# Kernel optimization log

Measured on AMD Instinct MI355X. Metric: run time of the kernel, lower is better.

## Reference

```python
import jax, jax.numpy as jnp
import numpy as np

B, S, E, FF = 8, 16384, 256, 1024
H, W, G = 128, 128, 16
Hn, Wn = H // G, W // G


def setup_inputs() -> dict:
    key = jax.random.key(0)
    ks = jax.random.split(key, 16)
    w = lambda k, shape: jax.random.normal(k, shape, jnp.float32) * 0.02
    return {
        "x": jax.random.normal(ks[0], (B, S, E), jnp.float32),
        "Wq": w(ks[1], (E, E)), "bq": jnp.zeros((E,), jnp.float32),
        "Wk": w(ks[2], (E, E)), "bk": jnp.zeros((E,), jnp.float32),
        "Wv": w(ks[3], (E, E)), "bv": jnp.zeros((E,), jnp.float32),
        "Wo": w(ks[4], (E, E)), "bo": jnp.zeros((E,), jnp.float32),
        "W1": w(ks[5], (E, FF)), "b1": jnp.zeros((FF,), jnp.float32),
        "W2": w(ks[6], (FF, E)), "b2": jnp.zeros((E,), jnp.float32),
        "g1": jnp.ones((E,), jnp.float32), "be1": jnp.zeros((E,), jnp.float32),
        "g2": jnp.ones((E,), jnp.float32), "be2": jnp.zeros((E,), jnp.float32),
    }


def _ln(x, g, b, eps=1e-5):
    m = jnp.mean(x, axis=-1, keepdims=True)
    v = jnp.mean(jnp.square(x - m), axis=-1, keepdims=True)
    return (x - m) * jax.lax.rsqrt(v + eps) * g + b


def _forward(x, Wq, bq, Wk, bk, Wv, bv, Wo, bo, W1, b1, W2, b2, g1, be1, g2, be2):
    # x: (B, S, E) -> (B, E, H, W), faithful to torch reshape (row-major reinterpret)
    x4 = x.reshape(B, E, H, W)
    # window partition: each window is the contiguous (E, G, G) block the torch loop slices
    xw = x4.reshape(B, E, Hn, G, Wn, G).transpose(0, 2, 4, 1, 3, 5)  # (B,Hn,Wn,E,G,G)
    # faithful raw reinterpretation (E,G,G) -> (G*G, E), matching grid.reshape(B,-1,E)
    t = xw.reshape(B, Hn * Wn, G * G, E)  # (B, nW, T=256, E)
    # single-head self-attention per window (batched over all windows at once)
    q = jnp.einsum('bwte,ef->bwtf', t, Wq) + bq
    k = jnp.einsum('bwte,ef->bwtf', t, Wk) + bk
    v = jnp.einsum('bwte,ef->bwtf', t, Wv) + bv
    scores = jnp.einsum('bwqe,bwke->bwqk', q, k) / jnp.sqrt(jnp.float32(E))
    attn = jax.nn.softmax(scores, axis=-1)
    o = jnp.einsum('bwqk,bwke->bwqe', attn, v)
    o = jnp.einsum('bwte,ef->bwtf', o, Wo) + bo  # (B, nW, 256, E)
    # reverse: view each window back to (E,G,G) and reassemble the feature map
    y = o.reshape(B, Hn, Wn, E, G, G).transpose(0, 3, 1, 4, 2, 5).reshape(B, E, H, W)
    y = y.reshape(B, S, E)  # faithful x.view(B, -1, E)
    # FFN (dropout is identity in eval) + residual with post-LN as written
    h = jax.nn.gelu(jnp.einsum('bse,ef->bsf', y, W1) + b1, approximate=False)
    ffn = jnp.einsum('bsf,fe->bse', h, W2) + b2
    y = y + _ln(ffn, g1, be1)
    y = y + _ln(y, g2, be2)
    return y


def reference(x, Wq, bq, Wk, bk, Wv, bv, Wo, bo, W1, b1, W2, b2, g1, be1, g2, be2):
    return _forward(x, Wq, bq, Wk, bk, Wv, bv, Wo, bo, W1, b1, W2, b2, g1, be1, g2, be2)
```

## Files before the change

### kernel.cpp

```cpp
#include <hip/hip_runtime.h>
#include <hip/hip_bf16.h>


typedef __bf16 bf16x8 __attribute__((ext_vector_type(8)));
typedef float  f32x4  __attribute__((ext_vector_type(4)));
typedef unsigned short us16;
typedef us16 us16x8 __attribute__((ext_vector_type(8)));
typedef us16 us16x4 __attribute__((ext_vector_type(4)));
typedef us16 us16x2 __attribute__((ext_vector_type(2)));

#define DI static __device__ __forceinline__

DI us16 f2b(float f){ __bf16 h = (__bf16)f; return __builtin_bit_cast(us16, h); }

DI bf16x8 cvt8(f32x4 a, f32x4 b){
  bf16x8 r;
  r[0]=(__bf16)a[0]; r[1]=(__bf16)a[1]; r[2]=(__bf16)a[2]; r[3]=(__bf16)a[3];
  r[4]=(__bf16)b[0]; r[5]=(__bf16)b[1]; r[6]=(__bf16)b[2]; r[7]=(__bf16)b[3];
  return r;
}
DI bf16x8 ld8(const us16* p){
  us16x8 v = *(const us16x8*)p;
  return __builtin_bit_cast(bf16x8, v);
}
DI f32x4 mfma16(bf16x8 a, bf16x8 b, f32x4 c){
  return __builtin_amdgcn_mfma_f32_16x16x32_bf16(a, b, c, 0, 0, 0);
}

DI bf16x8 ld_sw8(const char* base, int row, int f0){
  return ld8((const us16*)(base + row*512 + ((((f0>>3) ^ (row&7))) << 4)));
}
DI void st_sw1(char* base, int row, int f, us16 v){
  *(us16*)(base + row*512 + ((((f>>3) ^ (row&7))) << 4) + (f&7)*2) = v;
}
DI void st_sw4(char* base, int row, int f0, us16x4 v){
  *(us16x4*)(base + row*512 + ((((f0>>3) ^ (row&7))) << 4) + (f0&7)*2) = v;
}

DI bf16x8 ld_vt(const char* base, int row, int gg){
  return ld8((const us16*)(base + row*64 + (((gg ^ ((row>>1)&3))) << 4)));
}
DI void st_vt(char* base, int row, int col, us16 v){
  int c = col >> 3;
  *(us16*)(base + row*64 + (((c ^ ((row>>1)&3))) << 4) + (col&7)*2) = v;
}

DI void st_h1s(char* base, int row, int f, us16 v){
  *(us16*)(base + row*2048 + ((((f>>3) ^ (row&7))) << 4) + (f&7)*2) = v;
}
DI bf16x8 ld_h8s(const char* base, int row, int f0){
  return ld8((const us16*)(base + row*2048 + ((((f0>>3) ^ (row&7))) << 4)));
}

__global__ void prep_w(const float* __restrict__ src, us16* __restrict__ dst,
                       int R, int C, int cshift){
  int idx = blockIdx.x*256 + threadIdx.x;
  if(idx >= R*C) return;
  int r = idx >> cshift;
  int c = idx & (C-1);
  dst[(size_t)c*R + r] = f2b(src[idx]);
}

__global__ __launch_bounds__(256, 2)
void qkv_win(const float* __restrict__ x,
             const us16* __restrict__ WqT, const us16* __restrict__ WkT,
             const us16* __restrict__ WvT,
             const float* __restrict__ bq, const float* __restrict__ bk,
             const float* __restrict__ bv,
             char* __restrict__ Qimg, char* __restrict__ KV)
{
  __shared__ __align__(16) char smem[65536];
  const int tid = threadIdx.x;
  const int wl = tid >> 6, lane = tid & 63, l15 = lane & 15, g = lane >> 4;
  const int blk = blockIdx.x;
  const int hw = blk & 1, tg = (blk>>1)&7, wh = (blk>>4)&7, b = blk>>7;
  const int win = wh*8 + hw*4 + wl;

  {
    const float* xb = x + (size_t)b*4194304 + (size_t)(tg*32)*16384 + wh*2048 + hw*64;
    const int prow = tid >> 4, pc = tid & 15;
    char* abase = smem + (pc>>2)*16384;
    const int f0 = prow*16 + (pc&3)*4;
    for(int t=0; t<32; t++){
      f32x4 v = *(const f32x4*)(xb + (size_t)t*16384 + prow*128 + pc*4);
      us16x4 pk; pk[0]=f2b(v[0]); pk[1]=f2b(v[1]); pk[2]=f2b(v[2]); pk[3]=f2b(v[3]);
      st_sw4(abase, t, f0, pk);
    }
  }
  __syncthreads();
  bf16x8 tA[2][8];
  #pragma unroll
  for(int mi=0; mi<2; mi++)
    #pragma unroll
    for(int kk=0; kk<8; kk++)
      tA[mi][kk] = ld_sw8(smem + wl*16384, mi*16 + l15, kk*32 + g*8);
  __syncthreads();

  char* outb = smem + wl*16384;
  const size_t wslot = (size_t)(b*64 + win);

  for(int n0=0; n0<16; n0++){
    f32x4 a0 = {0,0,0,0}, a1 = {0,0,0,0};
    const us16* wrow = WqT + (size_t)(n0*16 + l15)*256;
    #pragma unroll
    for(int kk=0; kk<8; kk++){
      bf16x8 wb = ld8(wrow + kk*32 + g*8);
      a0 = mfma16(tA[0][kk], wb, a0);
      a1 = mfma16(tA[1][kk], wb, a1);
    }
    float bias = bq[n0*16 + l15];
    #pragma unroll
    for(int r=0; r<4; r++){
      st_sw1(outb, g*4+r,    n0*16+l15, f2b(a0[r] + bias));
      st_sw1(outb, 16+g*4+r, n0*16+l15, f2b(a1[r] + bias));
    }
  }
  asm volatile("" ::: "memory");
  {
    char* dst = Qimg + (wslot*8 + tg)*16384;
    #pragma unroll
    for(int i=0; i<16; i++)
      *(us16x8*)(dst + i*1024 + lane*16) = *(const us16x8*)(outb + i*1024 + lane*16);
  }
  asm volatile("" ::: "memory");

  for(int n0=0; n0<16; n0++){
    f32x4 a0 = {0,0,0,0}, a1 = {0,0,0,0};
    const us16* wrow = WkT + (size_t)(n0*16 + l15)*256;
    #pragma unroll
    for(int kk=0; kk<8; kk++){
      bf16x8 wb = ld8(wrow + kk*32 + g*8);
      a0 = mfma16(tA[0][kk], wb, a0);
      a1 = mfma16(tA[1][kk], wb, a1);
    }
    float bias = bk[n0*16 + l15];
    #pragma unroll
    for(int r=0; r<4; r++){
      st_sw1(outb, g*4+r,    n0*16+l15, f2b(a0[r] + bias));
      st_sw1(outb, 16+g*4+r, n0*16+l15, f2b(a1[r] + bias));
    }
  }
  asm volatile("" ::: "memory");
  {
    char* dst = KV + wslot*262144 + tg*16384;
    #pragma unroll
    for(int i=0; i<16; i++)
      *(us16x8*)(dst + i*1024 + lane*16) = *(const us16x8*)(outb + i*1024 + lane*16);
  }
  asm volatile("" ::: "memory");

  for(int n0=0; n0<16; n0++){
    f32x4 a0 = {0,0,0,0}, a1 = {0,0,0,0};
    const us16* wrow = WvT + (size_t)(n0*16 + l15)*256;
    f32x4 bv4 = *(const f32x4*)(bv + n0*16 + g*4);
    #pragma unroll
    for(int kk=0; kk<8; kk++){
      bf16x8 wa = ld8(wrow + kk*32 + g*8);
      a0 = mfma16(wa, tA[0][kk], a0);
      a1 = mfma16(wa, tA[1][kk], a1);
    }
    #pragma unroll
    for(int r=0; r<4; r++){
      int jr = n0*16 + g*4 + r;
      st_vt(outb, jr, l15,      f2b(a0[r] + bv4[r]));
      st_vt(outb, jr, 16 + l15, f2b(a1[r] + bv4[r]));
    }
  }
  asm volatile("" ::: "memory");
  {
    char* dst = KV + wslot*262144 + 131072 + tg*16384;
    #pragma unroll
    for(int i=0; i<16; i++)
      *(us16x8*)(dst + i*1024 + lane*16) = *(const us16x8*)(outb + i*1024 + lane*16);
  }
}

__global__ __launch_bounds__(256, 2)
void kv_win(const float* __restrict__ x,
            const us16* __restrict__ WkT, const us16* __restrict__ WvT,
            const float* __restrict__ bk, const float* __restrict__ bv,
            char* __restrict__ KV)
{
  __shared__ __align__(16) char smem[65536];
  const int tid = threadIdx.x;
  const int wl = tid >> 6, lane = tid & 63, l15 = lane & 15, g = lane >> 4;
  const int blk = blockIdx.x;
  const int hw = blk & 1, tg = (blk>>1)&7, wh = (blk>>4)&7, b = blk>>7;
  const int win = wh*8 + hw*4 + wl;

  {
    const float* xb = x + (size_t)b*4194304 + (size_t)(tg*32)*16384 + wh*2048 + hw*64;
    const int prow = tid >> 4, pc = tid & 15;
    char* abase = smem + (pc>>2)*16384;
    const int f0 = prow*16 + (pc&3)*4;
    for(int t=0; t<32; t++){
      f32x4 v = *(const f32x4*)(xb + (size_t)t*16384 + prow*128 + pc*4);
      us16x4 pk; pk[0]=f2b(v[0]); pk[1]=f2b(v[1]); pk[2]=f2b(v[2]); pk[3]=f2b(v[3]);
      st_sw4(abase, t, f0, pk);
    }
  }
  __syncthreads();
  bf16x8 tA[2][8];
  #pragma unroll
  for(int mi=0; mi<2; mi++)
    #pragma unroll
    for(int kk=0; kk<8; kk++)
      tA[mi][kk] = ld_sw8(smem + wl*16384, mi*16 + l15, kk*32 + g*8);
  __syncthreads();

  char* outb = smem + wl*16384;
  const size_t wslot = (size_t)(b*64 + win);

  for(int n0=0; n0<16; n0++){
    f32x4 a0 = {0,0,0,0}, a1 = {0,0,0,0};
    const us16* wrow = WkT + (size_t)(n0*16 + l15)*256;
    #pragma unroll
    for(int kk=0; kk<8; kk++){
      bf16x8 wb = ld8(wrow + kk*32 + g*8);
      a0 = mfma16(tA[0][kk], wb, a0);
      a1 = mfma16(tA[1][kk], wb, a1);
    }
    float bias = bk[n0*16 + l15];
    #pragma unroll
    for(int r=0; r<4; r++){
      st_sw1(outb, g*4+r,    n0*16+l15, f2b(a0[r] + bias));
      st_sw1(outb, 16+g*4+r, n0*16+l15, f2b(a1[r] + bias));
    }
  }
  asm volatile("" ::: "memory");
  {
    char* dst = KV + wslot*262144 + tg*16384;
    #pragma unroll
    for(int i=0; i<16; i++)
      *(us16x8*)(dst + i*1024 + lane*16) = *(const us16x8*)(outb + i*1024 + lane*16);
  }
  asm volatile("" ::: "memory");

  for(int n0=0; n0<16; n0++){
    f32x4 a0 = {0,0,0,0}, a1 = {0,0,0,0};
    const us16* wrow = WvT + (size_t)(n0*16 + l15)*256;
    f32x4 bv4 = *(const f32x4*)(bv + n0*16 + g*4);
    #pragma unroll
    for(int kk=0; kk<8; kk++){
      bf16x8 wa = ld8(wrow + kk*32 + g*8);
      a0 = mfma16(wa, tA[0][kk], a0);
      a1 = mfma16(wa, tA[1][kk], a1);
    }
    #pragma unroll
    for(int r=0; r<4; r++){
      int jr = n0*16 + g*4 + r;
      st_vt(outb, jr, l15,      f2b(a0[r] + bv4[r]));
      st_vt(outb, jr, 16 + l15, f2b(a1[r] + bv4[r]));
    }
  }
  asm volatile("" ::: "memory");
  {
    char* dst = KV + wslot*262144 + 131072 + tg*16384;
    #pragma unroll
    for(int i=0; i<16; i++)
      *(us16x8*)(dst + i*1024 + lane*16) = *(const us16x8*)(outb + i*1024 + lane*16);
  }
}

DI void load_kv_regs(const char* slot, int kt, us16x8* r, int wid, int lane){
  const char* src = (wid < 4)
      ? slot + (size_t)kt*16384 + wid*4096
      : slot + 131072 + (size_t)kt*16384 + (wid-4)*4096;
  #pragma unroll
  for(int i=0; i<4; i++)
    r[i] = *(const us16x8*)(src + i*1024 + lane*16);
}
DI void write_kv_lds(char* kb, char* vb, const us16x8* r, int wid, int lane){
  char* dst = (wid < 4) ? kb + wid*4096 : vb + (wid-4)*4096;
  #pragma unroll
  for(int i=0; i<4; i++)
    *(us16x8*)(dst + i*1024 + lane*16) = r[i];
}

DI void attn_core_loop(char* smem, us16* Psw, const char* slot,
                       const bf16x8 Qf[2][8], us16x8* stg,
                       const us16* WoT, const float* bo, float* yb,
                       int wid, int lane, int l15, int g, int r0)
{
  us16* Qw = (us16*)(smem) + wid*(32*264);
  float mr0 = -1e30f, mr1 = -1e30f, lr0 = 0.f, lr1 = 0.f;
  f32x4 Ot[16][2];
  const f32x4 zf = {0,0,0,0};
  #pragma unroll
  for(int i=0;i<16;i++){ Ot[i][0]=zf; Ot[i][1]=zf; }
  __syncthreads();

  for(int kt=0; kt<8; kt++){
    char* kb = (kt&1) ? smem + 16384 : smem;
    char* vb = (kt&1) ? smem + 49152 : smem + 32768;
    if(kt < 7) load_kv_regs(slot, kt+1, stg, wid, lane);
    f32x4 st[2][2] = {{zf,zf},{zf,zf}};
    #pragma unroll
    for(int kk=0; kk<8; kk++){
      int f0 = kk*32 + g*8;
      bf16x8 k0 = ld_sw8(kb, l15, f0);
      bf16x8 k1 = ld_sw8(kb, 16 + l15, f0);
      st[0][0] = mfma16(k0, Qf[0][kk], st[0][0]);
      st[0][1] = mfma16(k0, Qf[1][kk], st[0][1]);
      st[1][0] = mfma16(k1, Qf[0][kk], st[1][0]);
      st[1][1] = mfma16(k1, Qf[1][kk], st[1][1]);
    }
    #pragma unroll
    for(int mi=0; mi<2; mi++)
      #pragma unroll
      for(int qn=0; qn<2; qn++)
        #pragma unroll
        for(int r=0; r<4; r++) st[mi][qn][r] *= 0.0625f;
    float tm0 = st[0][0][0], tm1 = st[0][1][0];
    #pragma unroll
    for(int mi=0; mi<2; mi++)
      #pragma unroll
      for(int r=0; r<4; r++){
        tm0 = fmaxf(tm0, st[mi][0][r]);
        tm1 = fmaxf(tm1, st[mi][1][r]);
      }
    tm0 = fmaxf(tm0, __shfl_xor(tm0, 16)); tm0 = fmaxf(tm0, __shfl_xor(tm0, 32));
    tm1 = fmaxf(tm1, __shfl_xor(tm1, 16)); tm1 = fmaxf(tm1, __shfl_xor(tm1, 32));
    float mn0 = fmaxf(mr0, tm0), mn1 = fmaxf(mr1, tm1);
    float c0 = __expf(mr0 - mn0), c1 = __expf(mr1 - mn1);
    float ts0 = 0.f, ts1 = 0.f;
    #pragma unroll
    for(int mi=0; mi<2; mi++)
      #pragma unroll
      for(int r=0; r<4; r++){
        float p0 = __expf(st[mi][0][r] - mn0); st[mi][0][r] = p0; ts0 += p0;
        float p1 = __expf(st[mi][1][r] - mn1); st[mi][1][r] = p1; ts1 += p1;
      }
    ts0 += __shfl_xor(ts0, 16); ts0 += __shfl_xor(ts0, 32);
    ts1 += __shfl_xor(ts1, 16); ts1 += __shfl_xor(ts1, 32);
    lr0 = lr0*c0 + ts0;  lr1 = lr1*c1 + ts1;  mr0 = mn0;  mr1 = mn1;
    #pragma unroll
    for(int i=0;i<16;i++){
      #pragma unroll
      for(int r=0;r<4;r++){ Ot[i][0][r] *= c0; Ot[i][1][r] *= c1; }
    }
    #pragma unroll
    for(int qn=0; qn<2; qn++)
      #pragma unroll
      for(int mi=0; mi<2; mi++)
        #pragma unroll
        for(int rp=0; rp<2; rp++){
          us16x2 pk;
          pk[0] = f2b(st[mi][qn][rp*2]);
          pk[1] = f2b(st[mi][qn][rp*2+1]);
          *(us16x2*)((char*)Psw + (qn*16 + l15)*80 + (mi*16 + g*4 + rp*2)*2) = pk;
        }
    asm volatile("" ::: "memory");
    bf16x8 pb0 = ld8(Psw + l15*40 + g*8);
    bf16x8 pb1 = ld8(Psw + (16 + l15)*40 + g*8);
    #pragma unroll
    for(int fm=0; fm<16; fm++){
      bf16x8 va = ld_vt(vb, fm*16 + l15, g);
      Ot[fm][0] = mfma16(va, pb0, Ot[fm][0]);
      Ot[fm][1] = mfma16(va, pb1, Ot[fm][1]);
    }
    if(kt < 7){
      char* kbn = (kt&1) ? smem : smem + 16384;
      char* vbn = (kt&1) ? smem + 32768 : smem + 49152;
      write_kv_lds(kbn, vbn, stg, wid, lane);
    }
    __syncthreads();
  }

  float inv0 = 1.f/lr0, inv1 = 1.f/lr1;
  #pragma unroll
  for(int fm=0; fm<16; fm++)
    #pragma unroll
    for(int rp=0; rp<2; rp++){
      us16x2 p0, p1;
      p0[0]=f2b(Ot[fm][0][rp*2]*inv0);   p0[1]=f2b(Ot[fm][0][rp*2+1]*inv0);
      p1[0]=f2b(Ot[fm][1][rp*2]*inv1);   p1[1]=f2b(Ot[fm][1][rp*2+1]*inv1);
      *(us16x2*)((char*)Qw + l15*528      + (fm*16 + g*4 + rp*2)*2) = p0;
      *(us16x2*)((char*)Qw + (16+l15)*528 + (fm*16 + g*4 + rp*2)*2) = p1;
    }
  asm volatile("" ::: "memory");
  bf16x8 Of[2][8];
  #pragma unroll
  for(int qm=0; qm<2; qm++)
    #pragma unroll
    for(int kk=0; kk<8; kk++)
      Of[qm][kk] = ld8(Qw + (qm*16 + l15)*264 + kk*32 + g*8);
  for(int n0=0; n0<16; n0++){
    f32x4 a0 = {0,0,0,0}, a1 = {0,0,0,0};
    const us16* wrow = WoT + (size_t)(n0*16 + l15)*256;
    #pragma unroll
    for(int kk=0; kk<8; kk++){
      bf16x8 wb = ld8(wrow + kk*32 + g*8);
      a0 = mfma16(Of[0][kk], wb, a0);
      a1 = mfma16(Of[1][kk], wb, a1);
    }
    float bias = bo[n0*16 + l15];
    #pragma unroll
    for(int r=0; r<4; r++){
      yb[(size_t)(r0 + g*4 + r)*16384      + n0*128 + l15] = a0[r] + bias;
      yb[(size_t)(r0 + 16 + g*4 + r)*16384 + n0*128 + l15] = a1[r] + bias;
    }
  }
}

__global__ __launch_bounds__(512, 2)
void attn_hyb2(const char* __restrict__ Qimg, const char* __restrict__ KV,
               const us16* __restrict__ WoT, const float* __restrict__ bo,
               float* __restrict__ y)
{
  __shared__ __align__(16) char smem[135168];
  const int tid = threadIdx.x, wid = tid>>6, lane = tid&63, l15 = lane&15, g = lane>>4;
  const int blk = blockIdx.x;
  const int b   = blk >> 6;
  const int win = blk & 63;
  const size_t base = (size_t)b*4194304 + (size_t)(win>>3)*2048 + (size_t)(win&7)*16;
  float*       yb = y + base;
  const char*  slot = KV + (size_t)blk*262144;
  const char*  Qt = Qimg + ((size_t)blk*8 + wid)*16384;
  us16* Psw = (us16*)(smem + 65536) + wid*1280;
  const int r0 = wid*32;

  us16x8 stg[4];
  load_kv_regs(slot, 0, stg, wid, lane);

  bf16x8 Qf[2][8];
  #pragma unroll
  for(int qn=0; qn<2; qn++)
    #pragma unroll
    for(int kk=0; kk<8; kk++){
      int row = qn*16 + l15;
      Qf[qn][kk] = ld8((const us16*)(Qt + row*512 + ((((kk*4+g) ^ (l15&7))) << 4)));
    }

  write_kv_lds(smem, smem + 32768, stg, wid, lane);
  attn_core_loop(smem, Psw, slot, Qf, stg, WoT, bo, yb, wid, lane, l15, g, r0);
}

__global__ __launch_bounds__(512, 2)
void attn_hyb(const float* __restrict__ x,
              const us16* __restrict__ WqT, const float* __restrict__ bq,
              const char* __restrict__ KV,
              const us16* __restrict__ WoT, const float* __restrict__ bo,
              float* __restrict__ y)
{
  __shared__ __align__(16) char smem[135168];
  const int tid = threadIdx.x, wid = tid>>6, lane = tid&63, l15 = lane&15, g = lane>>4;
  const int blk = blockIdx.x;
  const int b   = blk >> 6;
  const int win = blk & 63;
  const size_t base = (size_t)b*4194304 + (size_t)(win>>3)*2048 + (size_t)(win&7)*16;
  const float* xb = x + base;
  float*       yb = y + base;
  const char*  slot = KV + (size_t)blk*262144;

  us16* Qw  = (us16*)(smem) + wid*(32*264);
  us16* Psw = (us16*)(smem + 65536) + wid*1280;
  const int r0 = wid*32;

  us16x8 stg[4];
  load_kv_regs(slot, 0, stg, wid, lane);

  bf16x8 tA[2][8];
  #pragma unroll
  for(int mi=0; mi<2; mi++){
    const float* trow = xb + (size_t)(r0 + mi*16 + l15)*16384;
    #pragma unroll
    for(int kk=0; kk<8; kk++){
      int f0 = kk*32 + g*8;
      const float* p = trow + (f0>>4)*128 + (f0&15);
      tA[mi][kk] = cvt8(*(const f32x4*)p, *(const f32x4*)(p+4));
    }
  }
  for(int n0=0; n0<16; n0++){
    f32x4 a0 = {0,0,0,0}, a1 = {0,0,0,0};
    const us16* wrow = WqT + (size_t)(n0*16 + l15)*256;
    #pragma unroll
    for(int kk=0; kk<8; kk++){
      bf16x8 wb = ld8(wrow + kk*32 + g*8);
      a0 = mfma16(tA[0][kk], wb, a0);
      a1 = mfma16(tA[1][kk], wb, a1);
    }
    float bias = bq[n0*16 + l15];
    #pragma unroll
    for(int r=0; r<4; r++){
      Qw[(g*4+r)*264      + n0*16 + l15] = f2b(a0[r] + bias);
      Qw[(16+g*4+r)*264   + n0*16 + l15] = f2b(a1[r] + bias);
    }
  }
  asm volatile("" ::: "memory");
  bf16x8 Qf[2][8];
  #pragma unroll
  for(int qn=0; qn<2; qn++)
    #pragma unroll
    for(int kk=0; kk<8; kk++)
      Qf[qn][kk] = ld8(Qw + (qn*16 + l15)*264 + kk*32 + g*8);
  __syncthreads();

  write_kv_lds(smem, smem + 32768, stg, wid, lane);
  attn_core_loop(smem, Psw, slot, Qf, stg, WoT, bo, yb, wid, lane, l15, g, r0);
}

__global__ __launch_bounds__(512, 2)
void ffn_ln(float* y,
            const us16* __restrict__ W1T, const us16* __restrict__ W2T,
            const float* __restrict__ b1, const float* __restrict__ b2,
            const float* __restrict__ g1, const float* __restrict__ be1,
            const float* __restrict__ g2, const float* __restrict__ be2)
{
  __shared__ __align__(16) char smem[132096];
  us16*  h  = (us16*)smem;
  float* fl = (float*)smem;
  const int tid = threadIdx.x, wid = tid>>6, lane = tid&63, l15 = lane&15, g = lane>>4;
  float* Y = y + (size_t)blockIdx.x*64*256;

  bf16x8 ya[4][8];
  #pragma unroll
  for(int mi=0; mi<4; mi++){
    const float* p = Y + (size_t)(mi*16 + l15)*256;
    #pragma unroll
    for(int kk=0; kk<8; kk++){
      int f0 = kk*32 + g*8;
      ya[mi][kk] = cvt8(*(const f32x4*)(p + f0), *(const f32x4*)(p + f0 + 4));
    }
  }
  const f32x4 zf = {0,0,0,0};
  #pragma unroll 2
  for(int n0=0; n0<8; n0++){
    int j = wid*128 + n0*16 + l15;
    f32x4 acc[4] = {zf,zf,zf,zf};
    const us16* wrow = W1T + (size_t)j*256;
    #pragma unroll
    for(int kk=0; kk<8; kk++){
      bf16x8 wb = ld8(wrow + kk*32 + g*8);
      #pragma unroll
      for(int mi=0; mi<4; mi++) acc[mi] = mfma16(ya[mi][kk], wb, acc[mi]);
    }
    float bias = b1[j];
    #pragma unroll
    for(int mi=0; mi<4; mi++)
      #pragma unroll
      for(int r=0; r<4; r++){
        float v = acc[mi][r] + bias;
        v = 0.5f*v*(1.f + erff(v*0.70710678118654752f));
        h[(mi*16 + g*4 + r)*1032 + j] = f2b(v);
      }
  }
  __syncthreads();
  f32x4 acc2[4][2] = {{zf,zf},{zf,zf},{zf,zf},{zf,zf}};
  #pragma unroll 2
  for(int kk=0; kk<32; kk++){
    int f0 = kk*32 + g*8;
    bf16x8 ha[4];
    #pragma unroll
    for(int mi=0; mi<4; mi++) ha[mi] = ld8(h + (mi*16 + l15)*1032 + f0);
    #pragma unroll
    for(int n=0; n<2; n++){
      bf16x8 wb = ld8(W2T + (size_t)(wid*32 + n*16 + l15)*1024 + f0);
      #pragma unroll
      for(int mi=0; mi<4; mi++) acc2[mi][n] = mfma16(ha[mi], wb, acc2[mi][n]);
    }
  }
  __syncthreads();
  #pragma unroll
  for(int mi=0; mi<4; mi++)
    #pragma unroll
    for(int n=0; n<2; n++){
      float bias = b2[wid*32 + n*16 + l15];
      #pragma unroll
      for(int r=0; r<4; r++)
        fl[(mi*16 + g*4 + r)*260 + wid*32 + n*16 + l15] = acc2[mi][n][r] + bias;
    }
  __syncthreads();
  f32x4 G1  = *(const f32x4*)(g1  + lane*4);
  f32x4 BE1 = *(const f32x4*)(be1 + lane*4);
  f32x4 G2  = *(const f32x4*)(g2  + lane*4);
  f32x4 BE2 = *(const f32x4*)(be2 + lane*4);
  for(int rr=0; rr<8; rr++){
    int row = wid*8 + rr;
    f32x4 f  = *(const f32x4*)(fl + row*260 + lane*4);
    f32x4 yv = *(const f32x4*)(Y + (size_t)row*256 + lane*4);
    float s  = f[0]+f[1]+f[2]+f[3];
    float s2 = f[0]*f[0]+f[1]*f[1]+f[2]*f[2]+f[3]*f[3];
    #pragma unroll
    for(int m=1; m<=32; m<<=1){ s += __shfl_xor(s, m); s2 += __shfl_xor(s2, m); }
    float mu = s*(1.f/256.f);
    float rs = rsqrtf(fmaxf(s2*(1.f/256.f) - mu*mu, 0.f) + 1e-5f);
    f32x4 y1;
    #pragma unroll
    for(int i=0; i<4; i++) y1[i] = yv[i] + (f[i]-mu)*rs*G1[i] + BE1[i];
    float t1 = y1[0]+y1[1]+y1[2]+y1[3];
    float t2 = y1[0]*y1[0]+y1[1]*y1[1]+y1[2]*y1[2]+y1[3]*y1[3];
    #pragma unroll
    for(int m=1; m<=32; m<<=1){ t1 += __shfl_xor(t1, m); t2 += __shfl_xor(t2, m); }
    float mu2 = t1*(1.f/256.f);
    float rs2 = rsqrtf(fmaxf(t2*(1.f/256.f) - mu2*mu2, 0.f) + 1e-5f);
    f32x4 o;
    #pragma unroll
    for(int i=0; i<4; i++) o[i] = y1[i] + (y1[i]-mu2)*rs2*G2[i] + BE2[i];
    *(f32x4*)(Y + (size_t)row*256 + lane*4) = o;
  }
}

__global__ __launch_bounds__(512, 2)
void ffn_ln32s(float* y,
               const us16* __restrict__ W1T, const us16* __restrict__ W2T,
               const float* __restrict__ b1, const float* __restrict__ b2,
               const float* __restrict__ g1, const float* __restrict__ be1,
               const float* __restrict__ g2, const float* __restrict__ be2)
{
  __shared__ __align__(16) char smem[65536];
  float* fl = (float*)smem;
  const int tid = threadIdx.x, wid = tid>>6, lane = tid&63, l15 = lane&15, g = lane>>4;
  float* Y = y + (size_t)blockIdx.x*32*256;

  bf16x8 ya[2][8];
  #pragma unroll
  for(int mi=0; mi<2; mi++){
    const float* p = Y + (size_t)(mi*16 + l15)*256;
    #pragma unroll
    for(int kk=0; kk<8; kk++){
      int f0 = kk*32 + g*8;
      ya[mi][kk] = cvt8(*(const f32x4*)(p + f0), *(const f32x4*)(p + f0 + 4));
    }
  }
  const f32x4 zf = {0,0,0,0};
  for(int n0=0; n0<8; n0++){
    int j = wid*128 + n0*16 + l15;
    f32x4 acc[2] = {zf,zf};
    const us16* wrow = W1T + (size_t)j*256;
    #pragma unroll
    for(int kk=0; kk<8; kk++){
      bf16x8 wb = ld8(wrow + kk*32 + g*8);
      #pragma unroll
      for(int mi=0; mi<2; mi++) acc[mi] = mfma16(ya[mi][kk], wb, acc[mi]);
    }
    float bias = b1[j];
    #pragma unroll
    for(int mi=0; mi<2; mi++)
      #pragma unroll
      for(int r=0; r<4; r++){
        float v = acc[mi][r] + bias;
        v = 0.5f*v*(1.f + erff(v*0.70710678118654752f));
        st_h1s(smem, mi*16 + g*4 + r, j, f2b(v));
      }
  }
  __syncthreads();
  f32x4 acc2[2][2] = {{zf,zf},{zf,zf}};
  for(int kk=0; kk<32; kk++){
    int f0 = kk*32 + g*8;
    bf16x8 ha[2];
    #pragma unroll
    for(int mi=0; mi<2; mi++) ha[mi] = ld_h8s(smem, mi*16 + l15, f0);
    #pragma unroll
    for(int n=0; n<2; n++){
      bf16x8 wb = ld8(W2T + (size_t)(wid*32 + n*16 + l15)*1024 + f0);
      #pragma unroll
      for(int mi=0; mi<2; mi++) acc2[mi][n] = mfma16(ha[mi], wb, acc2[mi][n]);
    }
  }
  __syncthreads();
  #pragma unroll
  for(int mi=0; mi<2; mi++)
    #pragma unroll
    for(int n=0; n<2; n++){
      float bias = b2[wid*32 + n*16 + l15];
      #pragma unroll
      for(int r=0; r<4; r++)
        fl[(mi*16 + g*4 + r)*260 + wid*32 + n*16 + l15] = acc2[mi][n][r] + bias;
    }
  __syncthreads();
  f32x4 G1  = *(const f32x4*)(g1  + lane*4);
  f32x4 BE1 = *(const f32x4*)(be1 + lane*4);
  f32x4 G2  = *(const f32x4*)(g2  + lane*4);
  f32x4 BE2 = *(const f32x4*)(be2 + lane*4);
  for(int rr=0; rr<4; rr++){
    int row = wid*4 + rr;
    f32x4 f  = *(const f32x4*)(fl + row*260 + lane*4);
    f32x4 yv = *(const f32x4*)(Y + (size_t)row*256 + lane*4);
    float s  = f[0]+f[1]+f[2]+f[3];
    float s2 = f[0]*f[0]+f[1]*f[1]+f[2]*f[2]+f[3]*f[3];
    #pragma unroll
    for(int m=1; m<=32; m<<=1){ s += __shfl_xor(s, m); s2 += __shfl_xor(s2, m); }
    float mu = s*(1.f/256.f);
    float rs = rsqrtf(fmaxf(s2*(1.f/256.f) - mu*mu, 0.f) + 1e-5f);
    f32x4 y1;
    #pragma unroll
    for(int i=0; i<4; i++) y1[i] = yv[i] + (f[i]-mu)*rs*G1[i] + BE1[i];
    float t1 = y1[0]+y1[1]+y1[2]+y1[3];
    float t2 = y1[0]*y1[0]+y1[1]*y1[1]+y1[2]*y1[2]+y1[3]*y1[3];
    #pragma unroll
    for(int m=1; m<=32; m<<=1){ t1 += __shfl_xor(t1, m); t2 += __shfl_xor(t2, m); }
    float mu2 = t1*(1.f/256.f);
    float rs2 = rsqrtf(fmaxf(t2*(1.f/256.f) - mu2*mu2, 0.f) + 1e-5f);
    f32x4 o;
    #pragma unroll
    for(int i=0; i<4; i++) o[i] = y1[i] + (y1[i]-mu2)*rs2*G2[i] + BE2[i];
    *(f32x4*)(Y + (size_t)row*256 + lane*4) = o;
  }
}

__global__ __launch_bounds__(512, 2)
void attn_win(const float* __restrict__ x,
              const us16* __restrict__ WqT, const us16* __restrict__ WkT,
              const us16* __restrict__ WvT, const us16* __restrict__ WoT,
              const float* __restrict__ bq, const float* __restrict__ bk,
              const float* __restrict__ bv, const float* __restrict__ bo,
              float* __restrict__ y)
{
  __shared__ __align__(16) char smem[135168];
  const int tid = threadIdx.x;
  const int wid = tid >> 6;
  const int lane = tid & 63;
  const int l15 = lane & 15;
  const int g = lane >> 4;

  const int blk = blockIdx.x;
  const int b   = blk >> 6;
  const int win = blk & 63;
  const size_t base = (size_t)b*4194304 + (size_t)(win>>3)*2048 + (size_t)(win&7)*16;
  const float* xb = x + base;
  float*       yb = y + base;

  us16* Qw    = (us16*)(smem) + wid*(32*264);
  char* slabb = smem;
  char* kldsb = smem + 16384;
  us16* Vt    = (us16*)(smem + 32768);
  us16* Psw   = (us16*)(smem + 53248) + wid*1280;

  const int r0 = wid*32;

  bf16x8 tA[2][8];
  #pragma unroll
  for(int mi=0; mi<2; mi++){
    const float* trow = xb + (size_t)(r0 + mi*16 + l15)*16384;
    #pragma unroll
    for(int kk=0; kk<8; kk++){
      int f0 = kk*32 + g*8;
      const float* p = trow + (f0>>4)*128 + (f0&15);
      tA[mi][kk] = cvt8(*(const f32x4*)p, *(const f32x4*)(p+4));
    }
  }
  for(int n0=0; n0<16; n0++){
    f32x4 a0 = {0,0,0,0}, a1 = {0,0,0,0};
    const us16* wrow = WqT + (size_t)(n0*16 + l15)*256;
    #pragma unroll
    for(int kk=0; kk<8; kk++){
      bf16x8 wb = ld8(wrow + kk*32 + g*8);
      a0 = mfma16(tA[0][kk], wb, a0);
      a1 = mfma16(tA[1][kk], wb, a1);
    }
    float bias = bq[n0*16 + l15];
    #pragma unroll
    for(int r=0; r<4; r++){
      Qw[(g*4+r)*264      + n0*16 + l15] = f2b(a0[r] + bias);
      Qw[(16+g*4+r)*264   + n0*16 + l15] = f2b(a1[r] + bias);
    }
  }
  asm volatile("" ::: "memory");
  bf16x8 Qf[2][8];
  #pragma unroll
  for(int qn=0; qn<2; qn++)
    #pragma unroll
    for(int kk=0; kk<8; kk++)
      Qf[qn][kk] = ld8(Qw + (qn*16 + l15)*264 + kk*32 + g*8);
  __syncthreads();

  const float bkv0 = bk[wid*32 + l15], bkv1 = bk[wid*32 + 16 + l15];
  float bvv[2][4];
  #pragma unroll
  for(int m=0; m<2; m++)
    #pragma unroll
    for(int r=0; r<4; r++)
      bvv[m][r] = bv[wid*32 + m*16 + g*4 + r];

  float mr0 = -1e30f, mr1 = -1e30f, lr0 = 0.f, lr1 = 0.f;
  f32x4 Ot[16][2];
  const f32x4 zf = {0,0,0,0};
  #pragma unroll
  for(int i=0;i<16;i++){ Ot[i][0]=zf; Ot[i][1]=zf; }

  for(int kt=0; kt<8; kt++){
    const int kr0 = kt*32;
    {
      int row = tid >> 4, c = tid & 15;
      const float* trow = xb + (size_t)(kr0 + row)*16384;
      #pragma unroll
      for(int j=0; j<4; j++){
        int f0 = (c + 16*j)*4;
        const float* p = trow + (f0>>4)*128 + (f0&15);
        f32x4 v = *(const f32x4*)p;
        us16x4 pk; pk[0]=f2b(v[0]); pk[1]=f2b(v[1]); pk[2]=f2b(v[2]); pk[3]=f2b(v[3]);
        st_sw4(slabb, row, f0, pk);
      }
    }
    __syncthreads();
    {
      f32x4 acc[2][2] = {{zf,zf},{zf,zf}};
      #pragma unroll
      for(int kk=0; kk<8; kk++){
        int f0 = kk*32 + g*8;
        bf16x8 a0 = ld_sw8(slabb, l15, f0);
        bf16x8 a1 = ld_sw8(slabb, 16 + l15, f0);
        #pragma unroll
        for(int n=0; n<2; n++){
          bf16x8 wb = ld8(WkT + (size_t)(wid*32 + n*16 + l15)*256 + f0);
          acc[n][0] = mfma16(a0, wb, acc[n][0]);
          acc[n][1] = mfma16(a1, wb, acc[n][1]);
        }
      }
      #pragma unroll
      for(int n=0; n<2; n++){
        float bias = n ? bkv1 : bkv0;
        #pragma unroll
        for(int r=0; r<4; r++){
          st_sw1(kldsb, g*4+r,      wid*32 + n*16 + l15, f2b(acc[n][0][r] + bias));
          st_sw1(kldsb, 16+g*4+r,   wid*32 + n*16 + l15, f2b(acc[n][1][r] + bias));
        }
      }
    }
    {
      f32x4 acc[2][2] = {{zf,zf},{zf,zf}};
      #pragma unroll
      for(int kk=0; kk<8; kk++){
        int f0 = kk*32 + g*8;
        bf16x8 b0 = ld_sw8(slabb, l15, f0);
        bf16x8 b1 = ld_sw8(slabb, 16 + l15, f0);
        #pragma unroll
        for(int fm=0; fm<2; fm++){
          bf16x8 wa = ld8(WvT + (size_t)(wid*32 + fm*16 + l15)*256 + f0);
          acc[fm][0] = mfma16(wa, b0, acc[fm][0]);
          acc[fm][1] = mfma16(wa, b1, acc[fm][1]);
        }
      }
      #pragma unroll
      for(int fm=0; fm<2; fm++)
        #pragma unroll
        for(int n=0; n<2; n++)
          #pragma unroll
          for(int r=0; r<4; r++){
            int f = wid*32 + fm*16 + g*4 + r;
            Vt[f*40 + n*16 + l15] = f2b(acc[fm][n][r] + bvv[fm][r]);
          }
    }
    __syncthreads();
    f32x4 st[2][2] = {{zf,zf},{zf,zf}};
    #pragma unroll
    for(int kk=0; kk<8; kk++){
      int f0 = kk*32 + g*8;
      bf16x8 k0 = ld_sw8(kldsb, l15, f0);
      bf16x8 k1 = ld_sw8(kldsb, 16 + l15, f0);
      st[0][0] = mfma16(k0, Qf[0][kk], st[0][0]);
      st[0][1] = mfma16(k0, Qf[1][kk], st[0][1]);
      st[1][0] = mfma16(k1, Qf[0][kk], st[1][0]);
      st[1][1] = mfma16(k1, Qf[1][kk], st[1][1]);
    }
    #pragma unroll
    for(int mi=0; mi<2; mi++)
      #pragma unroll
      for(int qn=0; qn<2; qn++)
        #pragma unroll
        for(int r=0; r<4; r++) st[mi][qn][r] *= 0.0625f;
    float tm0 = st[0][0][0], tm1 = st[0][1][0];
    #pragma unroll
    for(int mi=0; mi<2; mi++)
      #pragma unroll
      for(int r=0; r<4; r++){
        tm0 = fmaxf(tm0, st[mi][0][r]);
        tm1 = fmaxf(tm1, st[mi][1][r]);
      }
    tm0 = fmaxf(tm0, __shfl_xor(tm0, 16)); tm0 = fmaxf(tm0, __shfl_xor(tm0, 32));
    tm1 = fmaxf(tm1, __shfl_xor(tm1, 16)); tm1 = fmaxf(tm1, __shfl_xor(tm1, 32));
    float mn0 = fmaxf(mr0, tm0), mn1 = fmaxf(mr1, tm1);
    float c0 = __expf(mr0 - mn0), c1 = __expf(mr1 - mn1);
    float ts0 = 0.f, ts1 = 0.f;
    #pragma unroll
    for(int mi=0; mi<2; mi++)
      #pragma unroll
      for(int r=0; r<4; r++){
        float p0 = __expf(st[mi][0][r] - mn0); st[mi][0][r] = p0; ts0 += p0;
        float p1 = __expf(st[mi][1][r] - mn1); st[mi][1][r] = p1; ts1 += p1;
      }
    ts0 += __shfl_xor(ts0, 16); ts0 += __shfl_xor(ts0, 32);
    ts1 += __shfl_xor(ts1, 16); ts1 += __shfl_xor(ts1, 32);
    lr0 = lr0*c0 + ts0;  lr1 = lr1*c1 + ts1;  mr0 = mn0;  mr1 = mn1;
    #pragma unroll
    for(int i=0;i<16;i++){
      #pragma unroll
      for(int r=0;r<4;r++){ Ot[i][0][r] *= c0; Ot[i][1][r] *= c1; }
    }
    #pragma unroll
    for(int qn=0; qn<2; qn++)
      #pragma unroll
      for(int mi=0; mi<2; mi++)
        #pragma unroll
        for(int rp=0; rp<2; rp++){
          us16x2 pk;
          pk[0] = f2b(st[mi][qn][rp*2]);
          pk[1] = f2b(st[mi][qn][rp*2+1]);
          *(us16x2*)((char*)Psw + (qn*16 + l15)*80 + (mi*16 + g*4 + rp*2)*2) = pk;
        }
    asm volatile("" ::: "memory");
    bf16x8 pb0 = ld8(Psw + l15*40 + g*8);
    bf16x8 pb1 = ld8(Psw + (16 + l15)*40 + g*8);
    #pragma unroll
    for(int fm=0; fm<16; fm++){
      bf16x8 va = ld8(Vt + (fm*16 + l15)*40 + g*8);
      Ot[fm][0] = mfma16(va, pb0, Ot[fm][0]);
      Ot[fm][1] = mfma16(va, pb1, Ot[fm][1]);
    }
    __syncthreads();
  }

  float inv0 = 1.f/lr0, inv1 = 1.f/lr1;
  #pragma unroll
  for(int fm=0; fm<16; fm++)
    #pragma unroll
    for(int rp=0; rp<2; rp++){
      us16x2 p0, p1;
      p0[0]=f2b(Ot[fm][0][rp*2]*inv0);   p0[1]=f2b(Ot[fm][0][rp*2+1]*inv0);
      p1[0]=f2b(Ot[fm][1][rp*2]*inv1);   p1[1]=f2b(Ot[fm][1][rp*2+1]*inv1);
      *(us16x2*)((char*)Qw + l15*528      + (fm*16 + g*4 + rp*2)*2) = p0;
      *(us16x2*)((char*)Qw + (16+l15)*528 + (fm*16 + g*4 + rp*2)*2) = p1;
    }
  asm volatile("" ::: "memory");
  bf16x8 Of[2][8];
  #pragma unroll
  for(int qm=0; qm<2; qm++)
    #pragma unroll
    for(int kk=0; kk<8; kk++)
      Of[qm][kk] = ld8(Qw + (qm*16 + l15)*264 + kk*32 + g*8);
  for(int n0=0; n0<16; n0++){
    f32x4 a0 = {0,0,0,0}, a1 = {0,0,0,0};
    const us16* wrow = WoT + (size_t)(n0*16 + l15)*256;
    #pragma unroll
    for(int kk=0; kk<8; kk++){
      bf16x8 wb = ld8(wrow + kk*32 + g*8);
      a0 = mfma16(Of[0][kk], wb, a0);
      a1 = mfma16(Of[1][kk], wb, a1);
    }
    float bias = bo[n0*16 + l15];
    #pragma unroll
    for(int r=0; r<4; r++){
      yb[(size_t)(r0 + g*4 + r)*16384      + n0*128 + l15] = a0[r] + bias;
      yb[(size_t)(r0 + 16 + g*4 + r)*16384 + n0*128 + l15] = a1[r] + bias;
    }
  }
}

extern "C" void kernel_launch(void* const* d_in, const int* in_sizes, int n_in,
                              void* d_out, int out_size, void* d_ws, size_t ws_size,
                              hipStream_t stream)
{
  const float* x   = (const float*)d_in[0];
  const float* Wq  = (const float*)d_in[1];
  const float* bq  = (const float*)d_in[2];
  const float* Wk  = (const float*)d_in[3];
  const float* bk  = (const float*)d_in[4];
  const float* Wv  = (const float*)d_in[5];
  const float* bv  = (const float*)d_in[6];
  const float* Wo  = (const float*)d_in[7];
  const float* bo  = (const float*)d_in[8];
  const float* W1  = (const float*)d_in[9];
  const float* b1  = (const float*)d_in[10];
  const float* W2  = (const float*)d_in[11];
  const float* b2  = (const float*)d_in[12];
  const float* g1  = (const float*)d_in[13];
  const float* be1 = (const float*)d_in[14];
  const float* g2  = (const float*)d_in[15];
  const float* be2 = (const float*)d_in[16];
  float* out = (float*)d_out;
  char* ws = (char*)d_ws;

  const size_t KVBYTES = 134217728ull;
  const size_t QBYTES  = 67108864ull;
  const size_t NEED_B  = KVBYTES + 1572864ull;
  const size_t NEED_A  = KVBYTES + QBYTES + 1572864ull;

  if(ws_size >= NEED_A){
    char* Qimg  = ws + KVBYTES;
    char* wbase = ws + KVBYTES + QBYTES;
    us16* WqT = (us16*)(wbase);
    us16* WkT = (us16*)(wbase + 131072);
    us16* WvT = (us16*)(wbase + 262144);
    us16* WoT = (us16*)(wbase + 393216);
    us16* W1T = (us16*)(wbase + 524288);
    us16* W2T = (us16*)(wbase + 1048576);

    prep_w<<<dim3(256),  dim3(256), 0, stream>>>(Wq, WqT, 256, 256, 8);
    prep_w<<<dim3(256),  dim3(256), 0, stream>>>(Wk, WkT, 256, 256, 8);
    prep_w<<<dim3(256),  dim3(256), 0, stream>>>(Wv, WvT, 256, 256, 8);
    prep_w<<<dim3(256),  dim3(256), 0, stream>>>(Wo, WoT, 256, 256, 8);
    prep_w<<<dim3(1024), dim3(256), 0, stream>>>(W1, W1T, 256, 1024, 10);
    prep_w<<<dim3(1024), dim3(256), 0, stream>>>(W2, W2T, 1024, 256, 8);

    qkv_win<<<dim3(1024), dim3(256), 0, stream>>>(x, WqT, WkT, WvT, bq, bk, bv,
                                                  Qimg, ws);
    attn_hyb2<<<dim3(512), dim3(512), 0, stream>>>(Qimg, ws, WoT, bo, out);
    ffn_ln<<<dim3(1024), dim3(512), 0, stream>>>(out, W1T, W2T, b1, b2,
                                                 g1, be1, g2, be2);
    ffn_ln32s<<<dim3(2048), dim3(512), 0, stream>>>(out + 16777216ull,
                                                    W1T, W2T, b1, b2,
                                                    g1, be1, g2, be2);
  } else if(ws_size >= NEED_B){
    char* wbase = ws + KVBYTES;
    us16* WqT = (us16*)(wbase);
    us16* WkT = (us16*)(wbase + 131072);
    us16* WvT = (us16*)(wbase + 262144);
    us16* WoT = (us16*)(wbase + 393216);
    us16* W1T = (us16*)(wbase + 524288);
    us16* W2T = (us16*)(wbase + 1048576);

    prep_w<<<dim3(256),  dim3(256), 0, stream>>>(Wq, WqT, 256, 256, 8);
    prep_w<<<dim3(256),  dim3(256), 0, stream>>>(Wk, WkT, 256, 256, 8);
    prep_w<<<dim3(256),  dim3(256), 0, stream>>>(Wv, WvT, 256, 256, 8);
    prep_w<<<dim3(256),  dim3(256), 0, stream>>>(Wo, WoT, 256, 256, 8);
    prep_w<<<dim3(1024), dim3(256), 0, stream>>>(W1, W1T, 256, 1024, 10);
    prep_w<<<dim3(1024), dim3(256), 0, stream>>>(W2, W2T, 1024, 256, 8);

    kv_win<<<dim3(1024), dim3(256), 0, stream>>>(x, WkT, WvT, bk, bv, ws);
    attn_hyb<<<dim3(512), dim3(512), 0, stream>>>(x, WqT, bq, ws, WoT, bo, out);
    ffn_ln<<<dim3(2048), dim3(512), 0, stream>>>(out, W1T, W2T, b1, b2,
                                                 g1, be1, g2, be2);
  } else {
    us16* WqT = (us16*)(ws);
    us16* WkT = (us16*)(ws + 131072);
    us16* WvT = (us16*)(ws + 262144);
    us16* WoT = (us16*)(ws + 393216);
    us16* W1T = (us16*)(ws + 524288);
    us16* W2T = (us16*)(ws + 1048576);

    prep_w<<<dim3(256),  dim3(256), 0, stream>>>(Wq, WqT, 256, 256, 8);
    prep_w<<<dim3(256),  dim3(256), 0, stream>>>(Wk, WkT, 256, 256, 8);
    prep_w<<<dim3(256),  dim3(256), 0, stream>>>(Wv, WvT, 256, 256, 8);
    prep_w<<<dim3(256),  dim3(256), 0, stream>>>(Wo, WoT, 256, 256, 8);
    prep_w<<<dim3(1024), dim3(256), 0, stream>>>(W1, W1T, 256, 1024, 10);
    prep_w<<<dim3(1024), dim3(256), 0, stream>>>(W2, W2T, 1024, 256, 8);

    attn_win<<<dim3(512), dim3(512), 0, stream>>>(x, WqT, WkT, WvT, WoT,
                                                  bq, bk, bv, bo, out);
    ffn_ln<<<dim3(2048), dim3(512), 0, stream>>>(out, W1T, W2T, b1, b2,
                                                 g1, be1, g2, be2);
  }
}
```

Measured before the change: 925.3 us.

## Chunk FFN hidden dimension to fuse W1/W2 per quarter with smaller LDS

Result: faster. 748.3 us, median of 2 (-19.1%).

```diff
diff --git a/kernel.cpp b/kernel.cpp
--- a/kernel.cpp
+++ b/kernel.cpp
@@ -43,13 +43,6 @@
 DI void st_vt(char* base, int row, int col, us16 v){
   int c = col >> 3;
   *(us16*)(base + row*64 + (((c ^ ((row>>1)&3))) << 4) + (col&7)*2) = v;
-}
-
-DI void st_h1s(char* base, int row, int f, us16 v){
-  *(us16*)(base + row*2048 + ((((f>>3) ^ (row&7))) << 4) + (f&7)*2) = v;
-}
-DI bf16x8 ld_h8s(const char* base, int row, int f0){
-  return ld8((const us16*)(base + row*2048 + ((((f0>>3) ^ (row&7))) << 4)));
 }
 
 __global__ void prep_w(const float* __restrict__ src, us16* __restrict__ dst,
@@ -501,6 +494,117 @@
 }
 
 __global__ __launch_bounds__(512, 2)
+void ffn_ln3s(float* y,
+              const us16* __restrict__ W1T, const us16* __restrict__ W2T,
+              const float* __restrict__ b1, const float* __restrict__ b2,
+              const float* __restrict__ g1, const float* __restrict__ be1,
+              const float* __restrict__ g2, const float* __restrict__ be2)
+{
+  __shared__ __align__(16) char smem[67584];
+  us16* tile = (us16*)smem;
+  us16* h    = (us16*)(smem + 33792);
+  float* fl  = (float*)smem;
+  const int tid = threadIdx.x, wid = tid>>6, lane = tid&63, l15 = lane&15, g = lane>>4;
+  float* Y = y + (size_t)blockIdx.x*64*256;
+
+  {
+    #pragma unroll
+    for(int rr=0; rr<8; rr++){
+      int row = wid*8 + rr;
+      f32x4 v = *(const f32x4*)(Y + (size_t)row*256 + lane*4);
+      us16x4 pk; pk[0]=f2b(v[0]); pk[1]=f2b(v[1]); pk[2]=f2b(v[2]); pk[3]=f2b(v[3]);
+      *(us16x4*)(tile + row*264 + lane*4) = pk;
+    }
+  }
+  __syncthreads();
+
+  const f32x4 zf = {0,0,0,0};
+  f32x4 acc2[4][2] = {{zf,zf},{zf,zf},{zf,zf},{zf,zf}};
+  for(int q=0; q<4; q++){
+    f32x4 acc[4][2] = {{zf,zf},{zf,zf},{zf,zf},{zf,zf}};
+    #pragma unroll
+    for(int kk=0; kk<8; kk++){
+      int f0 = kk*32 + g*8;
+      bf16x8 ya[4];
+      #pragma unroll
+      for(int mi=0; mi<4; mi++) ya[mi] = ld8(tile + (mi*16 + l15)*264 + f0);
+      #pragma unroll
+      for(int n=0; n<2; n++){
+        bf16x8 wb = ld8(W1T + (size_t)(q*256 + wid*32 + n*16 + l15)*256 + f0);
+        #pragma unroll
+        for(int mi=0; mi<4; mi++) acc[mi][n] = mfma16(ya[mi], wb, acc[mi][n]);
+      }
+    }
+    #pragma unroll
+    for(int n=0; n<2; n++){
+      int jl = wid*32 + n*16 + l15;
+      float bias = b1[q*256 + jl];
+      #pragma unroll
+      for(int mi=0; mi<4; mi++)
+        #pragma unroll
+        for(int r=0; r<4; r++){
+          float v = acc[mi][n][r] + bias;
+          v = 0.5f*v*(1.f + erff(v*0.70710678118654752f));
+          h[(mi*16 + g*4 + r)*264 + jl] = f2b(v);
+        }
+    }
+    __syncthreads();
+    #pragma unroll
+    for(int kk=0; kk<8; kk++){
+      int f0 = kk*32 + g*8;
+      bf16x8 ha[4];
+      #pragma unroll
+      for(int mi=0; mi<4; mi++) ha[mi] = ld8(h + (mi*16 + l15)*264 + f0);
+      #pragma unroll
+      for(int n=0; n<2; n++){
+        bf16x8 wb = ld8(W2T + (size_t)(wid*32 + n*16 + l15)*1024 + q*256 + f0);
+        #pragma unroll
+        for(int mi=0; mi<4; mi++) acc2[mi][n] = mfma16(ha[mi], wb, acc2[mi][n]);
+      }
+    }
+    __syncthreads();
+  }
+  #pragma unroll
+  for(int n=0; n<2; n++){
+    float bias = b2[wid*32 + n*16 + l15];
+    #pragma unroll
+    for(int mi=0; mi<4; mi++)
+      #pragma unroll
+      for(int r=0; r<4; r++)
+        fl[(mi*16 + g*4 + r)*260 + wid*32 + n*16 + l15] = acc2[mi][n][r] + bias;
+  }
+  __syncthreads();
+  f32x4 G1  = *(const f32x4*)(g1  + lane*4);
+  f32x4 BE1 = *(const f32x4*)(be1 + lane*4);
+  f32x4 G2  = *(const f32x4*)(g2  + lane*4);
+  f32x4 BE2 = *(const f32x4*)(be2 + lane*4);
+  for(int rr=0; rr<8; rr++){
+    int row = wid*8 + rr;
+    f32x4 f  = *(const f32x4*)(fl + row*260 + lane*4);
+    f32x4 yv = *(const f32x4*)(Y + (size_t)row*256 + lane*4);
+    float s  = f[0]+f[1]+f[2]+f[3];
+    float s2 = f[0]*f[0]+f[1]*f[1]+f[2]*f[2]+f[3]*f[3];
+    #pragma unroll
+    for(int m=1; m<=32; m<<=1){ s += __shfl_xor(s, m); s2 += __shfl_xor(s2, m); }
+    float mu = s*(1.f/256.f);
+    float rs = rsqrtf(fmaxf(s2*(1.f/256.f) - mu*mu, 0.f) + 1e-5f);
+    f32x4 y1;
+    #pragma unroll
+    for(int i=0; i<4; i++) y1[i] = yv[i] + (f[i]-mu)*rs*G1[i] + BE1[i];
+    float t1 = y1[0]+y1[1]+y1[2]+y1[3];
+    float t2 = y1[0]*y1[0]+y1[1]*y1[1]+y1[2]*y1[2]+y1[3]*y1[3];
+    #pragma unroll
+    for(int m=1; m<=32; m<<=1){ t1 += __shfl_xor(t1, m); t2 += __shfl_xor(t2, m); }
+    float mu2 = t1*(1.f/256.f);
+    float rs2 = rsqrtf(fmaxf(t2*(1.f/256.f) - mu2*mu2, 0.f) + 1e-5f);
+    f32x4 o;
+    #pragma unroll
+    for(int i=0; i<4; i++) o[i] = y1[i] + (y1[i]-mu2)*rs2*G2[i] + BE2[i];
+    *(f32x4*)(Y + (size_t)row*256 + lane*4) = o;
+  }
+}
+
+__global__ __launch_bounds__(512, 2)
 void ffn_ln(float* y,
             const us16* __restrict__ W1T, const us16* __restrict__ W2T,
             const float* __restrict__ b1, const float* __restrict__ b2,
@@ -577,104 +681,6 @@
   f32x4 BE2 = *(const f32x4*)(be2 + lane*4);
   for(int rr=0; rr<8; rr++){
     int row = wid*8 + rr;
-    f32x4 f  = *(const f32x4*)(fl + row*260 + lane*4);
-    f32x4 yv = *(const f32x4*)(Y + (size_t)row*256 + lane*4);
-    float s  = f[0]+f[1]+f[2]+f[3];
-    float s2 = f[0]*f[0]+f[1]*f[1]+f[2]*f[2]+f[3]*f[3];
-    #pragma unroll
-    for(int m=1; m<=32; m<<=1){ s += __shfl_xor(s, m); s2 += __shfl_xor(s2, m); }
-    float mu = s*(1.f/256.f);
-    float rs = rsqrtf(fmaxf(s2*(1.f/256.f) - mu*mu, 0.f) + 1e-5f);
-    f32x4 y1;
-    #pragma unroll
-    for(int i=0; i<4; i++) y1[i] = yv[i] + (f[i]-mu)*rs*G1[i] + BE1[i];
-    float t1 = y1[0]+y1[1]+y1[2]+y1[3];
-    float t2 = y1[0]*y1[0]+y1[1]*y1[1]+y1[2]*y1[2]+y1[3]*y1[3];
-    #pragma unroll
-    for(int m=1; m<=32; m<<=1){ t1 += __shfl_xor(t1, m); t2 += __shfl_xor(t2, m); }
-    float mu2 = t1*(1.f/256.f);
-    float rs2 = rsqrtf(fmaxf(t2*(1.f/256.f) - mu2*mu2, 0.f) + 1e-5f);
-    f32x4 o;
-    #pragma unroll
-    for(int i=0; i<4; i++) o[i] = y1[i] + (y1[i]-mu2)*rs2*G2[i] + BE2[i];
-    *(f32x4*)(Y + (size_t)row*256 + lane*4) = o;
-  }
-}
-
-__global__ __launch_bounds__(512, 2)
-void ffn_ln32s(float* y,
-               const us16* __restrict__ W1T, const us16* __restrict__ W2T,
-               const float* __restrict__ b1, const float* __restrict__ b2,
-               const float* __restrict__ g1, const float* __restrict__ be1,
-               const float* __restrict__ g2, const float* __restrict__ be2)
-{
-  __shared__ __align__(16) char smem[65536];
-  float* fl = (float*)smem;
-  const int tid = threadIdx.x, wid = tid>>6, lane = tid&63, l15 = lane&15, g = lane>>4;
-  float* Y = y + (size_t)blockIdx.x*32*256;
-
-  bf16x8 ya[2][8];
-  #pragma unroll
-  for(int mi=0; mi<2; mi++){
-    const float* p = Y + (size_t)(mi*16 + l15)*256;
-    #pragma unroll
-    for(int kk=0; kk<8; kk++){
-      int f0 = kk*32 + g*8;
-      ya[mi][kk] = cvt8(*(const f32x4*)(p + f0), *(const f32x4*)(p + f0 + 4));
-    }
-  }
-  const f32x4 zf = {0,0,0,0};
-  for(int n0=0; n0<8; n0++){
-    int j = wid*128 + n0*16 + l15;
-    f32x4 acc[2] = {zf,zf};
-    const us16* wrow = W1T + (size_t)j*256;
-    #pragma unroll
-    for(int kk=0; kk<8; kk++){
-      bf16x8 wb = ld8(wrow + kk*32 + g*8);
-      #pragma unroll
-      for(int mi=0; mi<2; mi++) acc[mi] = mfma16(ya[mi][kk], wb, acc[mi]);
-    }
-    float bias = b1[j];
-    #pragma unroll
-    for(int mi=0; mi<2; mi++)
-      #pragma unroll
-      for(int r=0; r<4; r++){
-        float v = acc[mi][r] + bias;
-        v = 0.5f*v*(1.f + erff(v*0.70710678118654752f));
-        st_h1s(smem, mi*16 + g*4 + r, j, f2b(v));
-      }
-  }
-  __syncthreads();
-  f32x4 acc2[2][2] = {{zf,zf},{zf,zf}};
-  for(int kk=0; kk<32; kk++){
-    int f0 = kk*32 + g*8;
-    bf16x8 ha[2];
-    #pragma unroll
-    for(int mi=0; mi<2; mi++) ha[mi] = ld_h8s(smem, mi*16 + l15, f0);
-    #pragma unroll
-    for(int n=0; n<2; n++){
-      bf16x8 wb = ld8(W2T + (size_t)(wid*32 + n*16 + l15)*1024 + f0);
-      #pragma unroll
-      for(int mi=0; mi<2; mi++) acc2[mi][n] = mfma16(ha[mi], wb, acc2[mi][n]);
-    }
-  }
-  __syncthreads();
-  #pragma unroll
-  for(int mi=0; mi<2; mi++)
-    #pragma unroll
-    for(int n=0; n<2; n++){
-      float bias = b2[wid*32 + n*16 + l15];
-      #pragma unroll
-      for(int r=0; r<4; r++)
-        fl[(mi*16 + g*4 + r)*260 + wid*32 + n*16 + l15] = acc2[mi][n][r] + bias;
-    }
-  __syncthreads();
-  f32x4 G1  = *(const f32x4*)(g1  + lane*4);
-  f32x4 BE1 = *(const f32x4*)(be1 + lane*4);
-  f32x4 G2  = *(const f32x4*)(g2  + lane*4);
-  f32x4 BE2 = *(const f32x4*)(be2 + lane*4);
-  for(int rr=0; rr<4; rr++){
-    int row = wid*4 + rr;
     f32x4 f  = *(const f32x4*)(fl + row*260 + lane*4);
     f32x4 yv = *(const f32x4*)(Y + (size_t)row*256 + lane*4);
     float s  = f[0]+f[1]+f[2]+f[3];
@@ -996,11 +1002,8 @@
     qkv_win<<<dim3(1024), dim3(256), 0, stream>>>(x, WqT, WkT, WvT, bq, bk, bv,
                                                   Qimg, ws);
     attn_hyb2<<<dim3(512), dim3(512), 0, stream>>>(Qimg, ws, WoT, bo, out);
-    ffn_ln<<<dim3(1024), dim3(512), 0, stream>>>(out, W1T, W2T, b1, b2,
-                                                 g1, be1, g2, be2);
-    ffn_ln32s<<<dim3(2048), dim3(512), 0, stream>>>(out + 16777216ull,
-                                                    W1T, W2T, b1, b2,
-                                                    g1, be1, g2, be2);
+    ffn_ln3s<<<dim3(2048), dim3(512), 0, stream>>>(out, W1T, W2T, b1, b2,
+                                                   g1, be1, g2, be2);
   } else if(ws_size >= NEED_B){
     char* wbase = ws + KVBYTES;
     us16* WqT = (us16*)(wbase);
```
